# Performance work log

Measured on AMD Instinct MI355X. Metric: run time of the kernel, lower is better.

Reference implementation:

```python
import math
import jax, jax.numpy as jnp
import numpy as np

B, S, T, C, H = 4, 100, 128, 256, 256
NH, DH = 4, 32            # num_attention_heads//2, hidden_size//num_attention_heads
AH = NH * DH              # all_head_size = 128
FH = 32                   # fire_hidden_size
MAX_SP, MAX_TM, MAX_DOY = 180.0, 365.0, 182.0


def _fire(dist, c, w1, w2, max_dist):
    # FIREDistanceBias: log-compressed distance -> MLP(1->FH, SiLU, FH->1, no bias)
    c = jnp.maximum(c, 0.0)
    d = jnp.log(c * dist + 1.0) / jnp.log(c * max_dist + 1.0)
    h = jax.nn.silu(d[..., None] * w1[:, 0])   # (..., FH)
    return h @ w2[0]                            # (...,)


def setup_inputs() -> dict:
    key = jax.random.key(0)
    ks = jax.random.split(key, 20)
    p = 0.02
    inp = {
        "hidden_states": jax.random.normal(ks[0], (B, S, T, H), jnp.float32),
        "source_embeddings": jax.random.normal(ks[1], (B, S, C, H), jnp.float32),
        "attention_mask": jnp.zeros((B, 1, 1, T, C), jnp.float32),
        "st_dist": jax.random.uniform(ks[2], (B, T, C, 2), jnp.float32)
                   * jnp.array([MAX_SP, MAX_TM], jnp.float32),
        "st_doy_dist": jax.random.uniform(ks[3], (B, T, C), jnp.float32) * MAX_DOY,
        # attention projections (Linear H->AH with bias), output dense (AH->H)
        "Wq": jax.random.normal(ks[4], (AH, H), jnp.float32) * p,
        "bq": jnp.zeros((AH,), jnp.float32),
        "Wk": jax.random.normal(ks[5], (AH, H), jnp.float32) * p,
        "bk": jnp.zeros((AH,), jnp.float32),
        "Wv": jax.random.normal(ks[6], (AH, H), jnp.float32) * p,
        "bv": jnp.zeros((AH,), jnp.float32),
        "Wo": jax.random.normal(ks[7], (H, AH), jnp.float32) * p,
        "bo": jnp.zeros((H,), jnp.float32),
        # FIRE params: spatial / temporal / seasonal
        "c_s": jnp.float32(100.0),
        "w1_s": jax.random.normal(ks[8], (FH, 1), jnp.float32) * 0.5,
        "w2_s": jax.random.normal(ks[9], (1, FH), jnp.float32) * 0.5,
        "c_t": jnp.float32(100.0),
        "w1_t": jax.random.normal(ks[10], (FH, 1), jnp.float32) * 0.5,
        "w2_t": jax.random.normal(ks[11], (1, FH), jnp.float32) * 0.5,
        "c_d": jnp.float32(100.0),
        "w1_d": jax.random.normal(ks[12], (FH, 1), jnp.float32) * 0.5,
        "w2_d": jax.random.normal(ks[13], (1, FH), jnp.float32) * 0.5,
        # per-species log scales (init zeros in torch)
        "s_log_scale": jnp.zeros((S,), jnp.float32),
        "t_log_scale": jnp.zeros((S,), jnp.float32),
    }
    return inp


def reference(hidden_states, source_embeddings, attention_mask, st_dist, st_doy_dist,
              Wq, bq, Wk, bk, Wv, bv, Wo, bo,
              c_s, w1_s, w2_s, c_t, w1_t, w2_t, c_d, w1_d, w2_d,
              s_log_scale, t_log_scale):
    # FIRE distance biases over (B, T, C)
    sb = _fire(st_dist[..., 0], c_s, w1_s, w2_s, MAX_SP)
    tb = _fire(st_dist[..., 1], c_t, w1_t, w2_t, MAX_TM)
    db = _fire(st_doy_dist, c_d, w1_d, w2_d, MAX_DOY)
    # (B, S, T, C): species-scaled spatial+temporal + seasonal bias
    bias = (sb[:, None] * jnp.exp(s_log_scale)[None, :, None, None]
            + tb[:, None] * jnp.exp(t_log_scale)[None, :, None, None]
            + db[:, None])

    # projections; split heads: (B,S,L,AH) -> (B,S,NH,L,DH)
    q = (hidden_states @ Wq.T + bq).reshape(B, S, T, NH, DH).transpose(0, 1, 3, 2, 4)
    k = (source_embeddings @ Wk.T + bk).reshape(B, S, C, NH, DH).transpose(0, 1, 3, 2, 4)
    v = (source_embeddings @ Wv.T + bv).reshape(B, S, C, NH, DH).transpose(0, 1, 3, 2, 4)

    scores = jnp.einsum('bshtd,bshcd->bshtc', q, k) / math.sqrt(DH)
    scores = scores + attention_mask + bias[:, :, None]   # mask (B,1,1,T,C), bias (B,S,1,T,C)
    probs = jax.nn.softmax(scores, axis=-1)
    ctx = jnp.einsum('bshtc,bshcd->bshtd', probs, v)
    ctx = ctx.transpose(0, 1, 3, 2, 4).reshape(B, S, T, AH)
    return ctx @ Wo.T + bo   # STCrossOutput dense (dropout=0, eval)
```

## Files before the change

kernel.cpp:

```cpp
#include <hip/hip_runtime.h>
#include <hip/hip_bf16.h>
#include <math.h>

#define Bdim 4
#define Sdim 100
#define Tdim 128
#define Cdim 256
#define Hdim 256
#define NHd  4
#define DHd  32
#define AHd  128

typedef short bf16x8 __attribute__((ext_vector_type(8)));
typedef float f32x4 __attribute__((ext_vector_type(4)));

#define WAITCNT_V(n) do { \
  asm volatile("s_waitcnt vmcnt(" #n ")" ::: "memory"); \
  __builtin_amdgcn_sched_barrier(0); \
} while (0)

__device__ __forceinline__ short f2b(float x) {
  unsigned u = __float_as_uint(x);
  unsigned r = (u + 0x7FFF + ((u >> 16) & 1)) >> 16;
  return (short)r;
}

__device__ __forceinline__ void split2(float x, short& hi, short& lo) {
  unsigned u = __float_as_uint(x) & 0xFFFF0000u;
  hi = (short)(u >> 16);
  lo = f2b(x - __uint_as_float(u));
}

__device__ __forceinline__ float fire_eval(float dist, float c,
                                           const float* __restrict__ w1,
                                           const float* __restrict__ w2,
                                           float maxd) {
  c = fmaxf(c, 0.0f);
  float d = logf(fmaf(c, dist, 1.0f)) / logf(fmaf(c, maxd, 1.0f));
  float acc = 0.0f;
#pragma unroll
  for (int j = 0; j < 32; ++j) {
    float x = d * w1[j];
    float h = x / (1.0f + expf(-x));
    acc = fmaf(h, w2[j], acc);
  }
  return acc;
}

__global__ __launch_bounds__(256) void fire_bias_kernel(
    const float* __restrict__ st_dist, const float* __restrict__ st_doy,
    const float* __restrict__ mask,
    const float* __restrict__ c_s, const float* __restrict__ w1_s, const float* __restrict__ w2_s,
    const float* __restrict__ c_t, const float* __restrict__ w1_t, const float* __restrict__ w2_t,
    const float* __restrict__ c_d, const float* __restrict__ w1_d, const float* __restrict__ w2_d,
    float4* __restrict__ pk) {
  int i = blockIdx.x * 256 + threadIdx.x;
  if (i >= Bdim * Tdim * Cdim) return;
  float2 dv = ((const float2*)st_dist)[i];
  float4 r;
  r.x = fire_eval(dv.x, c_s[0], w1_s, w2_s, 180.0f);
  r.y = fire_eval(dv.y, c_t[0], w1_t, w2_t, 365.0f);
  r.z = fire_eval(st_doy[i], c_d[0], w1_d, w2_d, 182.0f) + mask[i];
  r.w = 0.0f;
  pk[i] = r;
}

__global__ __launch_bounds__(256) void bias_combine(
    const float4* __restrict__ pk,
    const float* __restrict__ sls, const float* __restrict__ tls,
    float* __restrict__ bF) {
  const int l = threadIdx.x & 63;
  const int lr = l & 15, lg = l >> 4;
  const int nt = blockIdx.x * 4 + (threadIdx.x >> 6);
  const int wt = blockIdx.y;
  const int b  = blockIdx.z;
  const int c = nt * 16 + lr;
  float sb[4], tb[4], db[4];
#pragma unroll
  for (int r = 0; r < 4; ++r) {
    float4 v = pk[(size_t)b * Tdim * Cdim + (size_t)(wt * 16 + lg * 4 + r) * Cdim + c];
    sb[r] = v.x; tb[r] = v.y; db[r] = v.z;
  }
  for (int s = 0; s < Sdim; ++s) {
    float es = __expf(sls[s]), et = __expf(tls[s]);
    float4 o;
    o.x = fmaf(sb[0], es, fmaf(tb[0], et, db[0]));
    o.y = fmaf(sb[1], es, fmaf(tb[1], et, db[1]));
    o.z = fmaf(sb[2], es, fmaf(tb[2], et, db[2]));
    o.w = fmaf(sb[3], es, fmaf(tb[3], et, db[3]));
    size_t idx = ((((size_t)(b * Sdim + s) * 8 + wt) * 16 + nt) * 64 + l);
    *(float4*)(bF + idx * 4) = o;
  }
}

__global__ __launch_bounds__(256) void wsplit_pack(
    const float* __restrict__ Wq, const float* __restrict__ Wk,
    const float* __restrict__ Wv, const float* __restrict__ Wo,
    short* __restrict__ pack) {
  int which = blockIdx.y;
  const float* W = which == 0 ? Wq : which == 1 ? Wk : which == 2 ? Wv : Wo;
  int idx = blockIdx.x * 256 + threadIdx.x;
  int j = idx & 7;
  int l = (idx >> 3) & 63;
  int frag = idx >> 9;
  int nt, kk8, Kd;
  if (which == 3) { nt = frag & 15; kk8 = frag >> 4; Kd = 128; }
  else           { nt = frag & 7;  kk8 = frag >> 3; Kd = 256; }
  int n = nt * 16 + (l & 15);
  int k = kk8 * 32 + (l >> 4) * 8 + j;
  float val = W[(size_t)n * Kd + k];
  short h, lo_;
  if (which == 3) split2(val, h, lo_);
  else { h = f2b(val); lo_ = 0; }
  pack[(size_t)which * 65536 + idx] = h;
  pack[(size_t)which * 65536 + 32768 + idx] = lo_;
}

__global__ __launch_bounds__(512, 4) void proj_q_mfma(
    const float* __restrict__ A, const short* __restrict__ Wp,
    const float* __restrict__ bias, short* __restrict__ O, float scale) {
  __shared__ short wlds[2][8 * 512];
  const int tid = threadIdx.x;
  const int l = tid & 63, w = tid >> 6;
  const int lr = l & 15, lg = l >> 4;
  const int m0 = blockIdx.x * 128;
  const int arow = m0 + w * 16 + lr;
  const float* ap = A + (size_t)arow * 256 + lg * 8;

  auto stage = [&](int buf, int kk) {
    const short* gsrc = Wp + ((size_t)(kk * 8 + w) * 64 + l) * 8;
    int loff = __builtin_amdgcn_readfirstlane(buf * 4096 + w * 512);
    __builtin_amdgcn_global_load_lds(gsrc, &wlds[0][0] + loff, 16, 0, 0);
  };

  f32x4 acc[8] = {};
  stage(0, 0);
  float4 ca = *(const float4*)ap;
  float4 cb = *(const float4*)(ap + 4);
#pragma unroll
  for (int kk = 0; kk < 8; ++kk) {
    const int buf = kk & 1;
    float4 na, nb;
    if (kk < 7) {
      stage(buf ^ 1, kk + 1);
      const float* np = ap + (kk + 1) * 32;
      na = *(const float4*)np;
      nb = *(const float4*)(np + 4);
    }
    float av[8] = {ca.x, ca.y, ca.z, ca.w, cb.x, cb.y, cb.z, cb.w};
    bf16x8 af;
#pragma unroll
    for (int e = 0; e < 8; ++e) af[e] = f2b(av[e]);
    if (kk < 7) { WAITCNT_V(3); } else { WAITCNT_V(0); }
    __builtin_amdgcn_s_barrier();
    const short* lb = &wlds[0][0] + buf * 4096 + l * 8;
#pragma unroll
    for (int nt = 0; nt < 8; ++nt) {
      bf16x8 wv = *(const bf16x8*)(lb + nt * 512);
      acc[nt] = __builtin_amdgcn_mfma_f32_16x16x32_bf16(af, wv, acc[nt], 0, 0, 0);
    }
    __builtin_amdgcn_s_barrier();
    if (kk < 7) { ca = na; cb = nb; }
  }
#pragma unroll
  for (int nt = 0; nt < 8; ++nt)
#pragma unroll
    for (int r = 0; r < 4; ++r)
      O[(size_t)(m0 + w * 16 + lg * 4 + r) * 128 + nt * 16 + lr] =
          f2b((acc[nt][r] + bias[nt * 16 + lr]) * scale);
}

__global__ __launch_bounds__(512, 4) void proj_kv_mfma(
    const float* __restrict__ A,
    const short* __restrict__ Wkp, const float* __restrict__ bk,
    const short* __restrict__ Wvp, const float* __restrict__ bv,
    short* __restrict__ Ko, short* __restrict__ Vo) {
  __shared__ short wlds[2][16 * 512];
  const int tid = threadIdx.x;
  const int l = tid & 63, w = tid >> 6;
  const int lr = l & 15, lg = l >> 4;
  const int m0 = blockIdx.x * 128;
  const int arow = m0 + w * 16 + lr;
  const float* ap = A + (size_t)arow * 256 + lg * 8;

  auto stage = [&](int buf, int kk) {
#pragma unroll
    for (int r = 0; r < 2; ++r) {
      int f = w + 8 * r;
      const short* gsrc = (r ? Wvp : Wkp) + ((size_t)(kk * 8 + w) * 64 + l) * 8;
      int loff = __builtin_amdgcn_readfirstlane(buf * 8192 + f * 512);
      __builtin_amdgcn_global_load_lds(gsrc, &wlds[0][0] + loff, 16, 0, 0);
    }
  };

  f32x4 accK[8] = {}, accV[8] = {};
  stage(0, 0);
  float4 ca = *(const float4*)ap;
  float4 cb = *(const float4*)(ap + 4);
#pragma unroll
  for (int kk = 0; kk < 8; ++kk) {
    const int buf = kk & 1;
    float4 na, nb;
    if (kk < 7) {
      stage(buf ^ 1, kk + 1);
      const float* np = ap + (kk + 1) * 32;
      na = *(const float4*)np;
      nb = *(const float4*)(np + 4);
    }
    float av[8] = {ca.x, ca.y, ca.z, ca.w, cb.x, cb.y, cb.z, cb.w};
    bf16x8 af;
#pragma unroll
    for (int e = 0; e < 8; ++e) af[e] = f2b(av[e]);
    if (kk < 7) { WAITCNT_V(4); } else { WAITCNT_V(0); }
    __builtin_amdgcn_s_barrier();
    const short* lb = &wlds[0][0] + buf * 8192 + l * 8;
#pragma unroll
    for (int nt = 0; nt < 8; ++nt) {
      bf16x8 kw = *(const bf16x8*)(lb + nt * 512);
      bf16x8 vw = *(const bf16x8*)(lb + (8 + nt) * 512);
      accK[nt] = __builtin_amdgcn_mfma_f32_16x16x32_bf16(af, kw, accK[nt], 0, 0, 0);
      accV[nt] = __builtin_amdgcn_mfma_f32_16x16x32_bf16(af, vw, accV[nt], 0, 0, 0);
    }
    __builtin_amdgcn_s_barrier();
    if (kk < 7) { ca = na; cb = nb; }
  }
#pragma unroll
  for (int nt = 0; nt < 8; ++nt)
#pragma unroll
    for (int r = 0; r < 4; ++r) {
      size_t row = (size_t)(m0 + w * 16 + lg * 4 + r) * 128 + nt * 16 + lr;
      Ko[row] = f2b(accK[nt][r] + bk[nt * 16 + lr]);
      Vo[row] = f2b(accV[nt][r] + bv[nt * 16 + lr]);
    }
}

__global__ __launch_bounds__(512, 4) void proj_o_mfma(
    const short* __restrict__ Ahi, const short* __restrict__ Alo,
    const short* __restrict__ Wp, const float* __restrict__ bias,
    float* __restrict__ O) {
  __shared__ short wlds[2][32 * 512];
  const int tid = threadIdx.x;
  const int l = tid & 63, w = tid >> 6;
  const int lr = l & 15, lg = l >> 4;
  const int m0 = blockIdx.x * 128;
  const int arow = m0 + w * 16 + lr;
  const short* ah = Ahi + (size_t)arow * 128 + lg * 8;
  const short* al = Alo + (size_t)arow * 128 + lg * 8;

  auto stage = [&](int buf, int kk) {
#pragma unroll
    for (int r = 0; r < 4; ++r) {
      int f = w + 8 * r;
      const short* gsrc = Wp + ((f >> 4) ? 32768 : 0)
                          + ((size_t)(kk * 16 + (f & 15)) * 64 + l) * 8;
      int loff = __builtin_amdgcn_readfirstlane(buf * 16384 + f * 512);
      __builtin_amdgcn_global_load_lds(gsrc, &wlds[0][0] + loff, 16, 0, 0);
    }
  };

  f32x4 acc[16] = {};
  stage(0, 0);
  bf16x8 cah = *(const bf16x8*)ah;
  bf16x8 cal = *(const bf16x8*)al;
#pragma unroll
  for (int kk = 0; kk < 4; ++kk) {
    const int buf = kk & 1;
    bf16x8 nah, nal;
    if (kk < 3) {
      stage(buf ^ 1, kk + 1);
      nah = *(const bf16x8*)(ah + (kk + 1) * 32);
      nal = *(const bf16x8*)(al + (kk + 1) * 32);
    }
    if (kk < 3) { WAITCNT_V(6); } else { WAITCNT_V(0); }
    __builtin_amdgcn_s_barrier();
    const short* lb = &wlds[0][0] + buf * 16384 + l * 8;
#pragma unroll
    for (int nt = 0; nt < 16; ++nt) {
      bf16x8 whi = *(const bf16x8*)(lb + nt * 512);
      bf16x8 wlo = *(const bf16x8*)(lb + (16 + nt) * 512);
      acc[nt] = __builtin_amdgcn_mfma_f32_16x16x32_bf16(cah, whi, acc[nt], 0, 0, 0);
      acc[nt] = __builtin_amdgcn_mfma_f32_16x16x32_bf16(cah, wlo, acc[nt], 0, 0, 0);
      acc[nt] = __builtin_amdgcn_mfma_f32_16x16x32_bf16(cal, whi, acc[nt], 0, 0, 0);
    }
    __builtin_amdgcn_s_barrier();
    if (kk < 3) { cah = nah; cal = nal; }
  }
#pragma unroll
  for (int nt = 0; nt < 16; ++nt)
#pragma unroll
    for (int r = 0; r < 4; ++r)
      O[(size_t)(m0 + w * 16 + lg * 4 + r) * 256 + nt * 16 + lr] =
          acc[nt][r] + bias[nt * 16 + lr];
}

__global__ __launch_bounds__(512, 2) void attn_mfma(
    const short* __restrict__ Qb, const short* __restrict__ Kb,
    const short* __restrict__ Vb,
    const float* __restrict__ bF,
    short* __restrict__ Chi, short* __restrict__ Clo) {
  __shared__ short vfrag[8][2][64][8];
  __shared__ short pbuf[8][16 * 36];

  const int tid = threadIdx.x;
  const int l = tid & 63;
  const int w = tid >> 6;
  const int lr = l & 15, lg = l >> 4;
  const int bid = blockIdx.x;
  const int xcd = bid & 7;
  const int i_  = bid >> 3;
  const int bs  = xcd * 50 + (i_ >> 2);
  const int h   = i_ & 3;

  const size_t kvbase = (size_t)bs * Cdim * AHd + h * DHd;
  const size_t qbase  = (size_t)bs * Tdim * AHd + h * DHd;

#pragma unroll
  for (int rep = 0; rep < 2; ++rep) {
    int chunk = tid * 2 + rep;
    int c = chunk >> 2, q = chunk & 3;
    bf16x8 v8 = *(const bf16x8*)(Vb + kvbase + (size_t)c * AHd + q * 8);
    int kc = c >> 5, nt = q >> 1;
    int lanebase = ((c & 31) >> 3) * 16 + (q & 1) * 8;
    int j = c & 7;
#pragma unroll
    for (int e = 0; e < 8; ++e) {
      int row = lanebase + e;
      int prow = row ^ ((row >> 4) << 1);
      vfrag[kc][nt][prow][j] = v8[e];
    }
  }
  __syncthreads();

  bf16x8 qf = *(const bf16x8*)(Qb + qbase + (size_t)(w * 16 + lr) * AHd + lg * 8);
  bf16x8 kf[16];
#pragma unroll
  for (int nt = 0; nt < 16; ++nt)
    kf[nt] = *(const bf16x8*)(Kb + kvbase + (size_t)(nt * 16 + lr) * AHd + lg * 8);

  const float4* bb = (const float4*)bF + ((size_t)bs * 8 + w) * 16 * 64 + l;
  f32x4 sacc[16];
#pragma unroll
  for (int nt = 0; nt < 16; ++nt) {
    float4 cv = bb[nt * 64];
    f32x4 cinit = {cv.x, cv.y, cv.z, cv.w};
    sacc[nt] = __builtin_amdgcn_mfma_f32_16x16x32_bf16(qf, kf[nt], cinit, 0, 0, 0);
  }

  float rinv[4];
#pragma unroll
  for (int nt = 0; nt < 16; ++nt)
#pragma unroll
    for (int r = 0; r < 4; ++r)
      sacc[nt][r] = __expf(sacc[nt][r]);
#pragma unroll
  for (int r = 0; r < 4; ++r) {
    float su = 0.f;
#pragma unroll
    for (int nt = 0; nt < 16; ++nt) su += sacc[nt][r];
#pragma unroll
    for (int off = 1; off < 16; off <<= 1) su += __shfl_xor(su, off);
    rinv[r] = 1.0f / su;
  }

  const f32x4 zero = {0.f, 0.f, 0.f, 0.f};
  f32x4 cacc[2] = {zero, zero};
  short* pb = &pbuf[w][0];
  const int lp = l ^ ((l >> 4) << 1);
#pragma unroll
  for (int kc = 0; kc < 8; ++kc) {
#pragma unroll
    for (int ntl = 0; ntl < 2; ++ntl) {
      int nt = kc * 2 + ntl;
#pragma unroll
      for (int r = 0; r < 4; ++r)
        pb[(lg * 4 + r) * 36 + ntl * 16 + lr] = f2b(sacc[nt][r]);
    }
    bf16x8 af = *(const bf16x8*)&pb[lr * 36 + lg * 8];
#pragma unroll
    for (int ntd = 0; ntd < 2; ++ntd) {
      bf16x8 vf = *(const bf16x8*)&vfrag[kc][ntd][lp][0];
      cacc[ntd] = __builtin_amdgcn_mfma_f32_16x16x32_bf16(af, vf, cacc[ntd], 0, 0, 0);
    }
  }

#pragma unroll
  for (int ntd = 0; ntd < 2; ++ntd)
#pragma unroll
    for (int r = 0; r < 4; ++r) {
      float val = cacc[ntd][r] * rinv[r];
      short h_, lo_;
      split2(val, h_, lo_);
      size_t idx = qbase + (size_t)(w * 16 + lg * 4 + r) * AHd + ntd * 16 + lr;
      Chi[idx] = h_;
      Clo[idx] = lo_;
    }
}

extern "C" void kernel_launch(void* const* d_in, const int* in_sizes, int n_in,
                              void* d_out, int out_size, void* d_ws, size_t ws_size,
                              hipStream_t stream) {
  const float* hs     = (const float*)d_in[0];
  const float* se     = (const float*)d_in[1];
  const float* mask   = (const float*)d_in[2];
  const float* stdist = (const float*)d_in[3];
  const float* stdoy  = (const float*)d_in[4];
  const float* Wq = (const float*)d_in[5];
  const float* bq = (const float*)d_in[6];
  const float* Wk = (const float*)d_in[7];
  const float* bk = (const float*)d_in[8];
  const float* Wv = (const float*)d_in[9];
  const float* bv = (const float*)d_in[10];
  const float* Wo = (const float*)d_in[11];
  const float* bo = (const float*)d_in[12];
  const float* c_s  = (const float*)d_in[13];
  const float* w1_s = (const float*)d_in[14];
  const float* w2_s = (const float*)d_in[15];
  const float* c_t  = (const float*)d_in[16];
  const float* w1_t = (const float*)d_in[17];
  const float* w2_t = (const float*)d_in[18];
  const float* c_d  = (const float*)d_in[19];
  const float* w1_d = (const float*)d_in[20];
  const float* w2_d = (const float*)d_in[21];
  const float* sls  = (const float*)d_in[22];
  const float* tls  = (const float*)d_in[23];
  float* out = (float*)d_out;

  float* ws = (float*)d_ws;
  const size_t BTC  = (size_t)Bdim * Tdim * Cdim;
  const size_t BSTC = (size_t)Bdim * Sdim * Tdim * Cdim;
  const size_t NQ   = (size_t)Bdim * Sdim * Tdim * AHd;
  const size_t NKV  = (size_t)Bdim * Sdim * Cdim * AHd;

  float4* pk  = (float4*)ws;
  float* bF   = ws + 4 * BTC;
  short* wpck = (short*)(bF + BSTC);
  short* Qb   = wpck + 262144;
  short* Kb   = Qb + NQ;
  short* Vb   = Kb + NKV;
  short* Chi  = Vb + NKV;
  short* Clo  = Chi + NQ;

  const int MQ  = Bdim * Sdim * Tdim;
  const int MKV = Bdim * Sdim * Cdim;

  fire_bias_kernel<<<(Bdim * Tdim * Cdim + 255) / 256, 256, 0, stream>>>(
      stdist, stdoy, mask, c_s, w1_s, w2_s, c_t, w1_t, w2_t, c_d, w1_d, w2_d, pk);

  bias_combine<<<dim3(4, 8, Bdim), 256, 0, stream>>>(pk, sls, tls, bF);

  wsplit_pack<<<dim3(128, 4), 256, 0, stream>>>(Wq, Wk, Wv, Wo, wpck);

  proj_q_mfma<<<dim3(MQ / 128), 512, 0, stream>>>(hs, wpck, bq, Qb,
                                                  0.17677669529663687f);
  proj_kv_mfma<<<dim3(MKV / 128), 512, 0, stream>>>(
      se, wpck + 65536, bk, wpck + 131072, bv, Kb, Vb);

  attn_mfma<<<dim3(Bdim * Sdim * NHd), 512, 0, stream>>>(
      Qb, Kb, Vb, bF, Chi, Clo);

  proj_o_mfma<<<dim3(MQ / 128), 512, 0, stream>>>(Chi, Clo, wpck + 196608, bo, out);
}
```

Measured before the change: 162.4 us.

## Merge Q/KV projections and bias combine into one launch; retile output projection

Merges the bias_combine, Q projection and KV projection kernels into a single phase1 launch that dispatches work by block index, so independent memory-bound and compute-bound work can overlap and launch gaps disappear. The output projection now uses 256-thread blocks where each wave computes two 16-row tiles, reusing each staged weight fragment across twice as many MFMAs. In the attention kernel, the Q/K global loads are hoisted above the V shuffle into LDS to overlap their latency. Risks are higher register pressure in proj_o and a less even block mix in phase1.

```diff
diff --git a/kernel.cpp b/kernel.cpp
--- a/kernel.cpp
+++ b/kernel.cpp
@@ -18,6 +18,8 @@
   asm volatile("s_waitcnt vmcnt(" #n ")" ::: "memory"); \
   __builtin_amdgcn_sched_barrier(0); \
 } while (0)
+
+#define MFMA16(a, b, c) __builtin_amdgcn_mfma_f32_16x16x32_bf16((a), (b), (c), 0, 0, 0)
 
 __device__ __forceinline__ short f2b(float x) {
   unsigned u = __float_as_uint(x);
@@ -63,34 +65,6 @@
   r.z = fire_eval(st_doy[i], c_d[0], w1_d, w2_d, 182.0f) + mask[i];
   r.w = 0.0f;
   pk[i] = r;
-}
-
-__global__ __launch_bounds__(256) void bias_combine(
-    const float4* __restrict__ pk,
-    const float* __restrict__ sls, const float* __restrict__ tls,
-    float* __restrict__ bF) {
-  const int l = threadIdx.x & 63;
-  const int lr = l & 15, lg = l >> 4;
-  const int nt = blockIdx.x * 4 + (threadIdx.x >> 6);
-  const int wt = blockIdx.y;
-  const int b  = blockIdx.z;
-  const int c = nt * 16 + lr;
-  float sb[4], tb[4], db[4];
-#pragma unroll
-  for (int r = 0; r < 4; ++r) {
-    float4 v = pk[(size_t)b * Tdim * Cdim + (size_t)(wt * 16 + lg * 4 + r) * Cdim + c];
-    sb[r] = v.x; tb[r] = v.y; db[r] = v.z;
-  }
-  for (int s = 0; s < Sdim; ++s) {
-    float es = __expf(sls[s]), et = __expf(tls[s]);
-    float4 o;
-    o.x = fmaf(sb[0], es, fmaf(tb[0], et, db[0]));
-    o.y = fmaf(sb[1], es, fmaf(tb[1], et, db[1]));
-    o.z = fmaf(sb[2], es, fmaf(tb[2], et, db[2]));
-    o.w = fmaf(sb[3], es, fmaf(tb[3], et, db[3]));
-    size_t idx = ((((size_t)(b * Sdim + s) * 8 + wt) * 16 + nt) * 64 + l);
-    *(float4*)(bF + idx * 4) = o;
-  }
 }
 
 __global__ __launch_bounds__(256) void wsplit_pack(
@@ -116,125 +90,151 @@
   pack[(size_t)which * 65536 + 32768 + idx] = lo_;
 }
 
-__global__ __launch_bounds__(512, 4) void proj_q_mfma(
-    const float* __restrict__ A, const short* __restrict__ Wp,
-    const float* __restrict__ bias, short* __restrict__ O, float scale) {
-  __shared__ short wlds[2][8 * 512];
+__global__ __launch_bounds__(512, 2) void phase1(
+    const float* __restrict__ se,
+    const short* __restrict__ Wkp, const float* __restrict__ bk,
+    const short* __restrict__ Wvp, const float* __restrict__ bv,
+    short* __restrict__ Ko, short* __restrict__ Vo,
+    const float* __restrict__ hs, const short* __restrict__ Wqp,
+    const float* __restrict__ bq, short* __restrict__ Qb, float scale,
+    const float4* __restrict__ pk,
+    const float* __restrict__ sls, const float* __restrict__ tls,
+    float* __restrict__ bF) {
+  __shared__ short wlds[2][16 * 512];
+  const int bid = blockIdx.x;
   const int tid = threadIdx.x;
   const int l = tid & 63, w = tid >> 6;
   const int lr = l & 15, lg = l >> 4;
-  const int m0 = blockIdx.x * 128;
-  const int arow = m0 + w * 16 + lr;
-  const float* ap = A + (size_t)arow * 256 + lg * 8;
-
-  auto stage = [&](int buf, int kk) {
-    const short* gsrc = Wp + ((size_t)(kk * 8 + w) * 64 + l) * 8;
-    int loff = __builtin_amdgcn_readfirstlane(buf * 4096 + w * 512);
-    __builtin_amdgcn_global_load_lds(gsrc, &wlds[0][0] + loff, 16, 0, 0);
-  };
-
-  f32x4 acc[8] = {};
-  stage(0, 0);
-  float4 ca = *(const float4*)ap;
-  float4 cb = *(const float4*)(ap + 4);
-#pragma unroll
-  for (int kk = 0; kk < 8; ++kk) {
-    const int buf = kk & 1;
-    float4 na, nb;
-    if (kk < 7) {
-      stage(buf ^ 1, kk + 1);
-      const float* np = ap + (kk + 1) * 32;
-      na = *(const float4*)np;
-      nb = *(const float4*)(np + 4);
-    }
-    float av[8] = {ca.x, ca.y, ca.z, ca.w, cb.x, cb.y, cb.z, cb.w};
-    bf16x8 af;
-#pragma unroll
-    for (int e = 0; e < 8; ++e) af[e] = f2b(av[e]);
-    if (kk < 7) { WAITCNT_V(3); } else { WAITCNT_V(0); }
-    __builtin_amdgcn_s_barrier();
-    const short* lb = &wlds[0][0] + buf * 4096 + l * 8;
-#pragma unroll
-    for (int nt = 0; nt < 8; ++nt) {
-      bf16x8 wv = *(const bf16x8*)(lb + nt * 512);
-      acc[nt] = __builtin_amdgcn_mfma_f32_16x16x32_bf16(af, wv, acc[nt], 0, 0, 0);
-    }
-    __builtin_amdgcn_s_barrier();
-    if (kk < 7) { ca = na; cb = nb; }
-  }
-#pragma unroll
-  for (int nt = 0; nt < 8; ++nt)
-#pragma unroll
-    for (int r = 0; r < 4; ++r)
-      O[(size_t)(m0 + w * 16 + lg * 4 + r) * 128 + nt * 16 + lr] =
-          f2b((acc[nt][r] + bias[nt * 16 + lr]) * scale);
-}
-
-__global__ __launch_bounds__(512, 4) void proj_kv_mfma(
-    const float* __restrict__ A,
-    const short* __restrict__ Wkp, const float* __restrict__ bk,
-    const short* __restrict__ Wvp, const float* __restrict__ bv,
-    short* __restrict__ Ko, short* __restrict__ Vo) {
-  __shared__ short wlds[2][16 * 512];
-  const int tid = threadIdx.x;
-  const int l = tid & 63, w = tid >> 6;
-  const int lr = l & 15, lg = l >> 4;
-  const int m0 = blockIdx.x * 128;
-  const int arow = m0 + w * 16 + lr;
-  const float* ap = A + (size_t)arow * 256 + lg * 8;
-
-  auto stage = [&](int buf, int kk) {
-#pragma unroll
-    for (int r = 0; r < 2; ++r) {
-      int f = w + 8 * r;
-      const short* gsrc = (r ? Wvp : Wkp) + ((size_t)(kk * 8 + w) * 64 + l) * 8;
-      int loff = __builtin_amdgcn_readfirstlane(buf * 8192 + f * 512);
-      __builtin_amdgcn_global_load_lds(gsrc, &wlds[0][0] + loff, 16, 0, 0);
-    }
-  };
-
-  f32x4 accK[8] = {}, accV[8] = {};
-  stage(0, 0);
-  float4 ca = *(const float4*)ap;
-  float4 cb = *(const float4*)(ap + 4);
-#pragma unroll
-  for (int kk = 0; kk < 8; ++kk) {
-    const int buf = kk & 1;
-    float4 na, nb;
-    if (kk < 7) {
-      stage(buf ^ 1, kk + 1);
-      const float* np = ap + (kk + 1) * 32;
-      na = *(const float4*)np;
-      nb = *(const float4*)(np + 4);
-    }
-    float av[8] = {ca.x, ca.y, ca.z, ca.w, cb.x, cb.y, cb.z, cb.w};
-    bf16x8 af;
-#pragma unroll
-    for (int e = 0; e < 8; ++e) af[e] = f2b(av[e]);
-    if (kk < 7) { WAITCNT_V(4); } else { WAITCNT_V(0); }
-    __builtin_amdgcn_s_barrier();
-    const short* lb = &wlds[0][0] + buf * 8192 + l * 8;
-#pragma unroll
-    for (int nt = 0; nt < 8; ++nt) {
-      bf16x8 kw = *(const bf16x8*)(lb + nt * 512);
-      bf16x8 vw = *(const bf16x8*)(lb + (8 + nt) * 512);
-      accK[nt] = __builtin_amdgcn_mfma_f32_16x16x32_bf16(af, kw, accK[nt], 0, 0, 0);
-      accV[nt] = __builtin_amdgcn_mfma_f32_16x16x32_bf16(af, vw, accV[nt], 0, 0, 0);
-    }
-    __builtin_amdgcn_s_barrier();
-    if (kk < 7) { ca = na; cb = nb; }
-  }
-#pragma unroll
-  for (int nt = 0; nt < 8; ++nt)
+
+  if (bid < 1200) {
+    const int g = bid / 3, m = bid - g * 3;
+    if (m < 2) {
+      const int m0 = (g * 2 + m) * 128;
+      const int arow = m0 + w * 16 + lr;
+      const float* ap = se + (size_t)arow * 256 + lg * 8;
+
+      auto stage = [&](int buf, int kk) {
+#pragma unroll
+        for (int r = 0; r < 2; ++r) {
+          int f = w + 8 * r;
+          const short* gsrc = (r ? Wvp : Wkp) + ((size_t)(kk * 8 + w) * 64 + l) * 8;
+          int loff = __builtin_amdgcn_readfirstlane(buf * 8192 + f * 512);
+          __builtin_amdgcn_global_load_lds(gsrc, &wlds[0][0] + loff, 16, 0, 0);
+        }
+      };
+
+      f32x4 accK[8] = {}, accV[8] = {};
+      stage(0, 0);
+      float4 ca = *(const float4*)ap;
+      float4 cb = *(const float4*)(ap + 4);
+#pragma unroll
+      for (int kk = 0; kk < 8; ++kk) {
+        const int buf = kk & 1;
+        float4 na, nb;
+        if (kk < 7) {
+          stage(buf ^ 1, kk + 1);
+          const float* np = ap + (kk + 1) * 32;
+          na = *(const float4*)np;
+          nb = *(const float4*)(np + 4);
+        }
+        float av[8] = {ca.x, ca.y, ca.z, ca.w, cb.x, cb.y, cb.z, cb.w};
+        bf16x8 af;
+#pragma unroll
+        for (int e = 0; e < 8; ++e) af[e] = f2b(av[e]);
+        if (kk < 7) { WAITCNT_V(4); } else { WAITCNT_V(0); }
+        __builtin_amdgcn_s_barrier();
+        const short* lb = &wlds[0][0] + buf * 8192 + l * 8;
+#pragma unroll
+        for (int nt = 0; nt < 8; ++nt) {
+          bf16x8 kw = *(const bf16x8*)(lb + nt * 512);
+          bf16x8 vw = *(const bf16x8*)(lb + (8 + nt) * 512);
+          accK[nt] = MFMA16(af, kw, accK[nt]);
+          accV[nt] = MFMA16(af, vw, accV[nt]);
+        }
+        __builtin_amdgcn_s_barrier();
+        if (kk < 7) { ca = na; cb = nb; }
+      }
+#pragma unroll
+      for (int nt = 0; nt < 8; ++nt)
+#pragma unroll
+        for (int r = 0; r < 4; ++r) {
+          size_t row = (size_t)(m0 + w * 16 + lg * 4 + r) * 128 + nt * 16 + lr;
+          Ko[row] = f2b(accK[nt][r] + bk[nt * 16 + lr]);
+          Vo[row] = f2b(accV[nt][r] + bv[nt * 16 + lr]);
+        }
+    } else {
+      const int m0 = g * 128;
+      const int arow = m0 + w * 16 + lr;
+      const float* ap = hs + (size_t)arow * 256 + lg * 8;
+
+      auto stage = [&](int buf, int kk) {
+        const short* gsrc = Wqp + ((size_t)(kk * 8 + w) * 64 + l) * 8;
+        int loff = __builtin_amdgcn_readfirstlane(buf * 8192 + w * 512);
+        __builtin_amdgcn_global_load_lds(gsrc, &wlds[0][0] + loff, 16, 0, 0);
+      };
+
+      f32x4 acc[8] = {};
+      stage(0, 0);
+      float4 ca = *(const float4*)ap;
+      float4 cb = *(const float4*)(ap + 4);
+#pragma unroll
+      for (int kk = 0; kk < 8; ++kk) {
+        const int buf = kk & 1;
+        float4 na, nb;
+        if (kk < 7) {
+          stage(buf ^ 1, kk + 1);
+          const float* np = ap + (kk + 1) * 32;
+          na = *(const float4*)np;
+          nb = *(const float4*)(np + 4);
+        }
+        float av[8] = {ca.x, ca.y, ca.z, ca.w, cb.x, cb.y, cb.z, cb.w};
+        bf16x8 af;
+#pragma unroll
+        for (int e = 0; e < 8; ++e) af[e] = f2b(av[e]);
+        if (kk < 7) { WAITCNT_V(3); } else { WAITCNT_V(0); }
+        __builtin_amdgcn_s_barrier();
+        const short* lb = &wlds[0][0] + buf * 8192 + l * 8;
+#pragma unroll
+        for (int nt = 0; nt < 8; ++nt) {
+          bf16x8 wv = *(const bf16x8*)(lb + nt * 512);
+          acc[nt] = MFMA16(af, wv, acc[nt]);
+        }
+        __builtin_amdgcn_s_barrier();
+        if (kk < 7) { ca = na; cb = nb; }
+      }
+#pragma unroll
+      for (int nt = 0; nt < 8; ++nt)
+#pragma unroll
+        for (int r = 0; r < 4; ++r)
+          Qb[(size_t)(m0 + w * 16 + lg * 4 + r) * 128 + nt * 16 + lr] =
+              f2b((acc[nt][r] + bq[nt * 16 + lr]) * scale);
+    }
+  } else {
+    const int bb_ = bid - 1200;
+    const int nt = (bb_ & 1) * 8 + w;
+    const int wt = (bb_ >> 1) & 7;
+    const int b  = bb_ >> 4;
+    const int c = nt * 16 + lr;
+    float sb[4], tb[4], db[4];
 #pragma unroll
     for (int r = 0; r < 4; ++r) {
-      size_t row = (size_t)(m0 + w * 16 + lg * 4 + r) * 128 + nt * 16 + lr;
-      Ko[row] = f2b(accK[nt][r] + bk[nt * 16 + lr]);
-      Vo[row] = f2b(accV[nt][r] + bv[nt * 16 + lr]);
-    }
-}
-
-__global__ __launch_bounds__(512, 4) void proj_o_mfma(
+      float4 v = pk[(size_t)b * Tdim * Cdim + (size_t)(wt * 16 + lg * 4 + r) * Cdim + c];
+      sb[r] = v.x; tb[r] = v.y; db[r] = v.z;
+    }
+    for (int s = 0; s < Sdim; ++s) {
+      float es = __expf(sls[s]), et = __expf(tls[s]);
+      float4 o;
+      o.x = fmaf(sb[0], es, fmaf(tb[0], et, db[0]));
+      o.y = fmaf(sb[1], es, fmaf(tb[1], et, db[1]));
+      o.z = fmaf(sb[2], es, fmaf(tb[2], et, db[2]));
+      o.w = fmaf(sb[3], es, fmaf(tb[3], et, db[3]));
+      size_t idx = ((((size_t)(b * Sdim + s) * 8 + wt) * 16 + nt) * 64 + l);
+      *(float4*)(bF + idx * 4) = o;
+    }
+  }
+}
+
+__global__ __launch_bounds__(256, 2) void proj_o_mfma(
     const short* __restrict__ Ahi, const short* __restrict__ Alo,
     const short* __restrict__ Wp, const float* __restrict__ bias,
     float* __restrict__ O) {
@@ -243,14 +243,15 @@
   const int l = tid & 63, w = tid >> 6;
   const int lr = l & 15, lg = l >> 4;
   const int m0 = blockIdx.x * 128;
-  const int arow = m0 + w * 16 + lr;
-  const short* ah = Ahi + (size_t)arow * 128 + lg * 8;
-  const short* al = Alo + (size_t)arow * 128 + lg * 8;
+  const short* ah0 = Ahi + (size_t)(m0 + w * 32 + lr) * 128 + lg * 8;
+  const short* al0 = Alo + (size_t)(m0 + w * 32 + lr) * 128 + lg * 8;
+  const short* ah1 = ah0 + (size_t)16 * 128;
+  const short* al1 = al0 + (size_t)16 * 128;
 
   auto stage = [&](int buf, int kk) {
 #pragma unroll
-    for (int r = 0; r < 4; ++r) {
-      int f = w + 8 * r;
+    for (int r = 0; r < 8; ++r) {
+      int f = w + 4 * r;
       const short* gsrc = Wp + ((f >> 4) ? 32768 : 0)
                           + ((size_t)(kk * 16 + (f & 15)) * 64 + l) * 8;
       int loff = __builtin_amdgcn_readfirstlane(buf * 16384 + f * 512);
@@ -258,39 +259,51 @@
     }
   };
 
-  f32x4 acc[16] = {};
+  f32x4 acc[2][16] = {};
   stage(0, 0);
-  bf16x8 cah = *(const bf16x8*)ah;
-  bf16x8 cal = *(const bf16x8*)al;
+  bf16x8 ch0 = *(const bf16x8*)ah0;
+  bf16x8 cl0 = *(const bf16x8*)al0;
+  bf16x8 ch1 = *(const bf16x8*)ah1;
+  bf16x8 cl1 = *(const bf16x8*)al1;
 #pragma unroll
   for (int kk = 0; kk < 4; ++kk) {
     const int buf = kk & 1;
-    bf16x8 nah, nal;
+    bf16x8 nh0, nl0, nh1, nl1;
     if (kk < 3) {
       stage(buf ^ 1, kk + 1);
-      nah = *(const bf16x8*)(ah + (kk + 1) * 32);
-      nal = *(const bf16x8*)(al + (kk + 1) * 32);
-    }
-    if (kk < 3) { WAITCNT_V(6); } else { WAITCNT_V(0); }
+      const int nk = (kk + 1) * 32;
+      nh0 = *(const bf16x8*)(ah0 + nk);
+      nl0 = *(const bf16x8*)(al0 + nk);
+      nh1 = *(const bf16x8*)(ah1 + nk);
+      nl1 = *(const bf16x8*)(al1 + nk);
+    }
+    if (kk < 3) { WAITCNT_V(12); } else { WAITCNT_V(0); }
     __builtin_amdgcn_s_barrier();
+    bf16x8 ahi[2] = {ch0, ch1};
+    bf16x8 alo[2] = {cl0, cl1};
     const short* lb = &wlds[0][0] + buf * 16384 + l * 8;
 #pragma unroll
     for (int nt = 0; nt < 16; ++nt) {
       bf16x8 whi = *(const bf16x8*)(lb + nt * 512);
       bf16x8 wlo = *(const bf16x8*)(lb + (16 + nt) * 512);
-      acc[nt] = __builtin_amdgcn_mfma_f32_16x16x32_bf16(cah, whi, acc[nt], 0, 0, 0);
-      acc[nt] = __builtin_amdgcn_mfma_f32_16x16x32_bf16(cah, wlo, acc[nt], 0, 0, 0);
-      acc[nt] = __builtin_amdgcn_mfma_f32_16x16x32_bf16(cal, whi, acc[nt], 0, 0, 0);
+#pragma unroll
+      for (int mi = 0; mi < 2; ++mi) {
+        acc[mi][nt] = MFMA16(ahi[mi], whi, acc[mi][nt]);
+        acc[mi][nt] = MFMA16(ahi[mi], wlo, acc[mi][nt]);
+        acc[mi][nt] = MFMA16(alo[mi], whi, acc[mi][nt]);
+      }
     }
     __builtin_amdgcn_s_barrier();
-    if (kk < 3) { cah = nah; cal = nal; }
-  }
-#pragma unroll
-  for (int nt = 0; nt < 16; ++nt)
-#pragma unroll
-    for (int r = 0; r < 4; ++r)
-      O[(size_t)(m0 + w * 16 + lg * 4 + r) * 256 + nt * 16 + lr] =
-          acc[nt][r] + bias[nt * 16 + lr];
+    if (kk < 3) { ch0 = nh0; cl0 = nl0; ch1 = nh1; cl1 = nl1; }
+  }
+#pragma unroll
+  for (int mi = 0; mi < 2; ++mi)
+#pragma unroll
+    for (int nt = 0; nt < 16; ++nt)
+#pragma unroll
+      for (int r = 0; r < 4; ++r)
+        O[(size_t)(m0 + w * 32 + mi * 16 + lg * 4 + r) * 256 + nt * 16 + lr] =
+            acc[mi][nt][r] + bias[nt * 16 + lr];
 }
 
 __global__ __launch_bounds__(512, 2) void attn_mfma(
@@ -314,6 +327,12 @@
   const size_t kvbase = (size_t)bs * Cdim * AHd + h * DHd;
   const size_t qbase  = (size_t)bs * Tdim * AHd + h * DHd;
 
+  bf16x8 qf = *(const bf16x8*)(Qb + qbase + (size_t)(w * 16 + lr) * AHd + lg * 8);
+  bf16x8 kf[16];
+#pragma unroll
+  for (int nt = 0; nt < 16; ++nt)
+    kf[nt] = *(const bf16x8*)(Kb + kvbase + (size_t)(nt * 16 + lr) * AHd + lg * 8);
+
 #pragma unroll
   for (int rep = 0; rep < 2; ++rep) {
     int chunk = tid * 2 + rep;
@@ -331,19 +350,13 @@
   }
   __syncthreads();
 
-  bf16x8 qf = *(const bf16x8*)(Qb + qbase + (size_t)(w * 16 + lr) * AHd + lg * 8);
-  bf16x8 kf[16];
-#pragma unroll
-  for (int nt = 0; nt < 16; ++nt)
-    kf[nt] = *(const bf16x8*)(Kb + kvbase + (size_t)(nt * 16 + lr) * AHd + lg * 8);
-
   const float4* bb = (const float4*)bF + ((size_t)bs * 8 + w) * 16 * 64 + l;
   f32x4 sacc[16];
 #pragma unroll
   for (int nt = 0; nt < 16; ++nt) {
     float4 cv = bb[nt * 64];
     f32x4 cinit = {cv.x, cv.y, cv.z, cv.w};
-    sacc[nt] = __builtin_amdgcn_mfma_f32_16x16x32_bf16(qf, kf[nt], cinit, 0, 0, 0);
+    sacc[nt] = MFMA16(qf, kf[nt], cinit);
   }
 
   float rinv[4];
@@ -379,7 +392,7 @@
 #pragma unroll
     for (int ntd = 0; ntd < 2; ++ntd) {
       bf16x8 vf = *(const bf16x8*)&vfrag[kc][ntd][lp][0];
-      cacc[ntd] = __builtin_amdgcn_mfma_f32_16x16x32_bf16(af, vf, cacc[ntd], 0, 0, 0);
+      cacc[ntd] = MFMA16(af, vf, cacc[ntd]);
     }
   }
 
@@ -441,22 +454,19 @@
   short* Clo  = Chi + NQ;
 
   const int MQ  = Bdim * Sdim * Tdim;
-  const int MKV = Bdim * Sdim * Cdim;
 
   fire_bias_kernel<<<(Bdim * Tdim * Cdim + 255) / 256, 256, 0, stream>>>(
       stdist, stdoy, mask, c_s, w1_s, w2_s, c_t, w1_t, w2_t, c_d, w1_d, w2_d, pk);
 
-  bias_combine<<<dim3(4, 8, Bdim), 256, 0, stream>>>(pk, sls, tls, bF);
-
   wsplit_pack<<<dim3(128, 4), 256, 0, stream>>>(Wq, Wk, Wv, Wo, wpck);
 
-  proj_q_mfma<<<dim3(MQ / 128), 512, 0, stream>>>(hs, wpck, bq, Qb,
-                                                  0.17677669529663687f);
-  proj_kv_mfma<<<dim3(MKV / 128), 512, 0, stream>>>(
-      se, wpck + 65536, bk, wpck + 131072, bv, Kb, Vb);
+  phase1<<<dim3(1264), 512, 0, stream>>>(
+      se, wpck + 65536, bk, wpck + 131072, bv, Kb, Vb,
+      hs, wpck, bq, Qb, 0.17677669529663687f,
+      pk, sls, tls, bF);
 
   attn_mfma<<<dim3(Bdim * Sdim * NHd), 512, 0, stream>>>(
       Qb, Kb, Vb, bF, Chi, Clo);
 
-  proj_o_mfma<<<dim3(MQ / 128), 512, 0, stream>>>(Chi, Clo, wpck + 196608, bo, out);
-}
+  proj_o_mfma<<<dim3(MQ / 128), 256, 0, stream>>>(Chi, Clo, wpck + 196608, bo, out);
+}
```

After: 160.3 us. Within noise of the previous version (-1.3%).
